# Performance work log

Hardware: AMD Instinct MI355X
Metric: run time of the kernel (lower is better)

## Reference

```python
import jax, jax.numpy as jnp
import numpy as np

B, SEQ, DIM = 4, 8192, 512
G = 32              # group_size: number of outer chunks (per source rearrange 'b (g n) d')
QK = 128            # query_key_dim
HD = QK // 4        # head_dim = 32 (used for softmax scale)
HEAD_D = 2 * HD     # per-head feature dim = 64 (h=2 heads over QK)
HID = DIM           # expansion_factor = 1.0
EPS = 1e-5


def _shift_seq(t):
    # F.pad(t, (0,0,1,-1)): prepend one zero row along axis=-2, drop last row
    pad = [(0, 0)] * (t.ndim - 2) + [(1, 0), (0, 0)]
    return jnp.pad(t, pad)[..., :-1, :]


def setup_inputs() -> dict:
    key = jax.random.key(0)
    ks = jax.random.split(key, 8)
    s = 0.02
    return {
        "x": jax.random.normal(ks[0], (B, SEQ, DIM), jnp.float32),
        "ln_g": jnp.ones((DIM,), jnp.float32),
        "ln_b": jnp.zeros((DIM,), jnp.float32),
        "w_qk": jax.random.normal(ks[1], (DIM, QK), jnp.float32) * s,
        "g4": jax.random.normal(ks[2], (4, QK), jnp.float32) * s,   # qk_offset_scale.gamma
        "b4": jnp.zeros((4, QK), jnp.float32),                       # qk_offset_scale.beta
        "g2": jax.random.normal(ks[3], (2, QK), jnp.float32) * s,   # shift_one_offset_scale.gamma
        "b2": jnp.zeros((2, QK), jnp.float32),
        "w_hidden": jax.random.normal(ks[4], (DIM, 2 * HID), jnp.float32) * s,
        "w_gate": jax.random.normal(ks[5], (DIM, HID), jnp.float32) * s,
        "w_out": jax.random.normal(ks[6], (5 * HID, DIM), jnp.float32) * s,
    }


def reference(x, ln_g, ln_b, w_qk, g4, b4, g2, b2, w_hidden, w_gate, w_out):
    b, seq, dim = x.shape
    n = seq // G  # tokens per chunk; seq chosen as multiple of G so padding = 0

    # LayerNorm
    mu = jnp.mean(x, axis=-1, keepdims=True)
    var = jnp.var(x, axis=-1, keepdims=True)
    xs = (x - mu) * jax.lax.rsqrt(var + EPS) * ln_g + ln_b

    # token shift of first half of channels (shift_tokens=True)
    half = dim // 2
    xs = jnp.concatenate([_shift_seq(xs[..., :half]), xs[..., half:]], axis=-1)

    qk = xs @ w_qk                                  # [b, seq, QK]
    qk_g = qk.reshape(b, G, n, QK)                  # 'b (g n) d -> b g n d', g outer
    qk_mean = qk_g.mean(axis=2)                     # [b, G, QK]

    # OffsetScale(heads=4) on per-chunk mean -> q_offset, k_offset, q_scale, k_scale
    offs = qk_mean[:, :, None, :] * g4 + b4         # [b, G, 4, QK]
    q_off, k_off, q_sc, k_sc = (offs[:, :, i, :] for i in range(4))

    q = qk_g * q_sc[:, :, None, :] + q_off[:, :, None, :]   # [b, G, n, QK]
    k = qk_g * k_sc[:, :, None, :] + k_off[:, :, None, :]

    # shift-by-one variants within each chunk, re-scaled + shift-one offsets
    q_s_off = qk_mean * g2[0] + b2[0]               # [b, G, QK]
    k_s_off = qk_mean * g2[1] + b2[1]
    qs = _shift_seq(q) * q_sc[:, :, None, :] + q_s_off[:, :, None, :]
    ks_ = _shift_seq(k) * k_sc[:, :, None, :] + k_s_off[:, :, None, :]

    def heads(t):  # [b,G,n,QK] -> [b,G,2,n,HEAD_D]
        return t.reshape(b, G, n, 2, HEAD_D).transpose(0, 1, 3, 2, 4)

    q_all = jnp.concatenate([heads(q), heads(qs)], axis=2)   # [b,G,4,n,64]
    k_all = jnp.concatenate([heads(k), heads(ks_)], axis=2)

    hg = xs @ w_hidden                              # [b, seq, 2*HID]
    hidden, gate = hg[..., :HID], hg[..., HID:]
    hidden_g = hidden.reshape(b, G, n, HID)

    sim = jnp.einsum('bghid,bghjd->bghij', q_all, k_all) * (HD ** -0.5)
    neg = -jnp.finfo(sim.dtype).max
    causal = jnp.triu(jnp.ones((n, n), dtype=bool), 1)  # applied unconditionally in source
    sim = jnp.where(causal, neg, sim)
    attn = jax.nn.softmax(sim, axis=-1)             # dropout=0 (eval)

    out = jnp.einsum('bghij,bgje->bghie', attn, hidden_g)   # [b,G,4,n,HID]
    gate_g = gate.reshape(b, G, n, HID)
    out = jax.nn.silu(out) * gate_g[:, :, None, :, :]
    out = out.transpose(0, 1, 3, 2, 4).reshape(b, seq, 4 * HID)  # 'b g h n e -> b (g n) (h e)'

    residual = jnp.concatenate([hidden, out], axis=-1)       # [b, seq, 5*HID]
    out = residual @ w_out                                   # [b, seq, dim]
    out = out * jax.nn.silu(xs @ w_gate)
    return out + xs
```

## Files before the change

### kernel.cpp

```cpp
#include <hip/hip_runtime.h>
#include <hip/hip_bf16.h>
#include <math.h>

#define BB 4
#define SEQ 8192
#define DIM 512
#define GG 32
#define NPG 256
#define QKD 128
#define HIDD 512

typedef unsigned short u16;
typedef unsigned int u32;

using s16x8 = __attribute__((ext_vector_type(8))) short;
using f32x4 = __attribute__((ext_vector_type(4))) float;

__device__ __forceinline__ float bf2f(u16 u) { return __uint_as_float(((u32)u) << 16); }
__device__ __forceinline__ u16 f2bf(float f) {
  u32 b = __float_as_uint(f);
  return (u16)((b + 0x7FFFu + ((b >> 16) & 1u)) >> 16);
}
__device__ __forceinline__ float silu_f(float x) { return x / (1.f + expf(-x)); }
__device__ __forceinline__ float silu_fast(float x) { return x / (1.f + __expf(-x)); }
__device__ __forceinline__ float4 fma4(float4 a, float4 b, float4 c) {
  return make_float4(a.x*b.x+c.x, a.y*b.y+c.y, a.z*b.z+c.z, a.w*b.w+c.w);
}
__device__ __forceinline__ float4 mul4(float4 a, float4 b) {
  return make_float4(a.x*b.x, a.y*b.y, a.z*b.z, a.w*b.w);
}
#define LD4(p, off) (*(const float4*)((p) + (off)))

__device__ __forceinline__ s16x8 aff8(s16x8 v, float4 s0, float4 s1, float4 o0, float4 o1) {
  union U { s16x8 x; u16 u[8]; };
  U in; in.x = v; U r;
  r.u[0] = f2bf(bf2f(in.u[0]) * s0.x + o0.x);
  r.u[1] = f2bf(bf2f(in.u[1]) * s0.y + o0.y);
  r.u[2] = f2bf(bf2f(in.u[2]) * s0.z + o0.z);
  r.u[3] = f2bf(bf2f(in.u[3]) * s0.w + o0.w);
  r.u[4] = f2bf(bf2f(in.u[4]) * s1.x + o1.x);
  r.u[5] = f2bf(bf2f(in.u[5]) * s1.y + o1.y);
  r.u[6] = f2bf(bf2f(in.u[6]) * s1.z + o1.z);
  r.u[7] = f2bf(bf2f(in.u[7]) * s1.w + o1.w);
  return r.x;
}
__device__ __forceinline__ s16x8 pack8(float4 a, float4 b) {
  union { s16x8 v; u16 u[8]; } z;
  z.u[0] = f2bf(a.x); z.u[1] = f2bf(a.y); z.u[2] = f2bf(a.z); z.u[3] = f2bf(a.w);
  z.u[4] = f2bf(b.x); z.u[5] = f2bf(b.y); z.u[6] = f2bf(b.z); z.u[7] = f2bf(b.w);
  return z.v;
}

__global__ __launch_bounds__(256) void k_ln(const float* __restrict__ x,
    const float* __restrict__ lg, const float* __restrict__ lb,
    float* __restrict__ xs, u16* __restrict__ xsb) {
  const int row = blockIdx.x;
  const int s = row & (SEQ - 1);
  const int t = threadIdx.x;
  const float* xr = x + (size_t)row * DIM;
  float v0 = xr[t], v1 = xr[t + 256];
  float sum = v0 + v1, sq = v0 * v0 + v1 * v1;
  #pragma unroll
  for (int o = 32; o; o >>= 1) { sum += __shfl_down(sum, o); sq += __shfl_down(sq, o); }
  __shared__ float sm[8];
  const int w = t >> 6;
  if ((t & 63) == 0) { sm[w] = sum; sm[4 + w] = sq; }
  __syncthreads();
  if (t == 0) {
    float S = sm[0] + sm[1] + sm[2] + sm[3];
    float Q = sm[4] + sm[5] + sm[6] + sm[7];
    float mu = S * (1.f / DIM);
    float var = Q * (1.f / DIM) - mu * mu;
    sm[0] = mu; sm[4] = rsqrtf(var + 1e-5f);
  }
  __syncthreads();
  const float mu = sm[0], rs = sm[4];
  float y0 = (v0 - mu) * rs * lg[t] + lb[t];
  float y1 = (v1 - mu) * rs * lg[t + 256] + lb[t + 256];
  xs[(size_t)row * DIM + t + 256] = y1;
  xsb[(size_t)row * DIM + t + 256] = f2bf(y1);
  if (s + 1 < SEQ) {
    xs[(size_t)(row + 1) * DIM + t] = y0;
    xsb[(size_t)(row + 1) * DIM + t] = f2bf(y0);
  }
  if (s == 0) { xs[(size_t)row * DIM + t] = 0.f; xsb[(size_t)row * DIM + t] = 0; }
}

__global__ __launch_bounds__(256) void k_trw(const float* __restrict__ src, u16* __restrict__ dst,
    int N, int dstLD, int rowOff) {
  __shared__ u16 T[64][66];
  const int t = threadIdx.x;
  const int k0 = blockIdx.x * 64, n0 = blockIdx.y * 64;
  #pragma unroll
  for (int i = 0; i < 16; ++i) {
    int idx = t + 256 * i;
    int r = idx >> 6, c = idx & 63;
    T[c][r] = f2bf(src[(size_t)(k0 + r) * N + n0 + c]);
  }
  __syncthreads();
  #pragma unroll
  for (int i = 0; i < 16; ++i) {
    int idx = t + 256 * i;
    int r = idx >> 6, c = idx & 63;
    dst[(size_t)(rowOff + n0 + r) * dstLD + k0 + c] = T[r][c];
  }
}

__global__ __launch_bounds__(256) void k_trh(const u16* __restrict__ hidt, u16* __restrict__ hidr) {
  __shared__ u16 T[64][66];
  const int t = threadIdx.x;
  const int j0 = blockIdx.x * 64;
  const int e0 = blockIdx.y * 64;
  const int bg = blockIdx.z;
  #pragma unroll
  for (int i = 0; i < 16; ++i) {
    int idx = t + 256 * i; int r = idx >> 6, c = idx & 63;
    T[c][r] = hidt[((size_t)bg * 512 + e0 + r) * 256 + j0 + c];
  }
  __syncthreads();
  #pragma unroll
  for (int i = 0; i < 16; ++i) {
    int idx = t + 256 * i; int r = idx >> 6, c = idx & 63;
    hidr[((size_t)bg * 256 + j0 + r) * 512 + e0 + c] = T[r][c];
  }
}

__global__ __launch_bounds__(256, 2) void k_gemm1m(const u16* __restrict__ xsb,
    const u16* __restrict__ w1t, u16* __restrict__ qk, u16* __restrict__ hidt,
    u16* __restrict__ gate, u16* __restrict__ xg) {
  __shared__ u16 As[2][128][72];
  __shared__ u16 Bs[2][128][72];
  const int t = threadIdx.x;
  const int blk = blockIdx.x;
  const int xcd = blk & 7;
  const int loc = blk >> 3;
  const int m0 = (xcd * 32 + loc / 13) * 128;
  const int n0 = (loc % 13) * 128;
  const int w = t >> 6, l = t & 63, lr = l & 15, lq = l >> 4;
  const int wr = (w >> 1) * 64, wc = (w & 1) * 64;
  const int sr = t >> 3;
  const int sk = (t & 7) * 8;
  f32x4 acc[4][4];
  #pragma unroll
  for (int i = 0; i < 4; ++i)
    #pragma unroll
    for (int j = 0; j < 4; ++j) acc[i][j] = (f32x4){0.f, 0.f, 0.f, 0.f};
  s16x8 rA[4], rB[4];
#define G1LOAD(T) { const int k0_ = (T) * 64;                                        \
    _Pragma("unroll")                                                                \
    for (int it = 0; it < 4; ++it) {                                                 \
      rA[it] = *(const s16x8*)(xsb + (size_t)(m0 + sr + it * 32) * 512 + k0_ + sk);  \
      rB[it] = *(const s16x8*)(w1t + (size_t)(n0 + sr + it * 32) * 512 + k0_ + sk);  \
    } }
  G1LOAD(0);
  #pragma unroll
  for (int it = 0; it < 4; ++it) {
    *(s16x8*)&As[0][sr + it * 32][sk] = rA[it];
    *(s16x8*)&Bs[0][sr + it * 32][sk] = rB[it];
  }
  G1LOAD(1);
  __syncthreads();
  for (int tt = 0; tt < 8; ++tt) {
    const int cur = tt & 1;
    if (tt + 1 < 8) {
      #pragma unroll
      for (int it = 0; it < 4; ++it) {
        *(s16x8*)&As[cur ^ 1][sr + it * 32][sk] = rA[it];
        *(s16x8*)&Bs[cur ^ 1][sr + it * 32][sk] = rB[it];
      }
      if (tt + 2 < 8) G1LOAD(tt + 2);
    }
    #pragma unroll
    for (int kk = 0; kk < 64; kk += 32) {
      s16x8 af[4], bf[4];
      #pragma unroll
      for (int fi = 0; fi < 4; ++fi) af[fi] = *(const s16x8*)&As[cur][wr + fi * 16 + lr][kk + 8 * lq];
      #pragma unroll
      for (int fj = 0; fj < 4; ++fj) bf[fj] = *(const s16x8*)&Bs[cur][wc + fj * 16 + lr][kk + 8 * lq];
      #pragma unroll
      for (int fi = 0; fi < 4; ++fi)
        #pragma unroll
        for (int fj = 0; fj < 4; ++fj)
          acc[fi][fj] = __builtin_amdgcn_mfma_f32_16x16x32_bf16(af[fi], bf[fj], acc[fi][fj], 0, 0, 0);
    }
    __syncthreads();
  }
#undef G1LOAD
  if (n0 == 0) {
    #pragma unroll
    for (int fi = 0; fi < 4; ++fi)
      #pragma unroll
      for (int fj = 0; fj < 4; ++fj) {
        const int n = wc + fj * 16 + lr;
        const int mb = m0 + wr + fi * 16 + lq * 4;
        #pragma unroll
        for (int r = 0; r < 4; ++r)
          qk[(size_t)(mb + r) * QKD + n] = f2bf(acc[fi][fj][r]);
      }
  } else if (n0 < 640) {
    const int bg = m0 >> 8;
    #pragma unroll
    for (int fi = 0; fi < 4; ++fi)
      #pragma unroll
      for (int fj = 0; fj < 4; ++fj) {
        const int e = n0 - 128 + wc + fj * 16 + lr;
        const int j0 = (m0 & 255) + wr + fi * 16 + lq * 4;
        ushort4 pk;
        pk.x = f2bf(acc[fi][fj][0]); pk.y = f2bf(acc[fi][fj][1]);
        pk.z = f2bf(acc[fi][fj][2]); pk.w = f2bf(acc[fi][fj][3]);
        *(ushort4*)(hidt + ((size_t)bg * 512 + e) * 256 + j0) = pk;
      }
  } else if (n0 < 1152) {
    #pragma unroll
    for (int fi = 0; fi < 4; ++fi)
      #pragma unroll
      for (int fj = 0; fj < 4; ++fj) {
        const int n = n0 - 640 + wc + fj * 16 + lr;
        const int mb = m0 + wr + fi * 16 + lq * 4;
        #pragma unroll
        for (int r = 0; r < 4; ++r)
          gate[(size_t)(mb + r) * HIDD + n] = f2bf(acc[fi][fj][r]);
      }
  } else {
    #pragma unroll
    for (int fi = 0; fi < 4; ++fi)
      #pragma unroll
      for (int fj = 0; fj < 4; ++fj) {
        const int n = n0 - 1152 + wc + fj * 16 + lr;
        const int mb = m0 + wr + fi * 16 + lq * 4;
        #pragma unroll
        for (int r = 0; r < 4; ++r)
          xg[(size_t)(mb + r) * HIDD + n] = f2bf(silu_f(acc[fi][fj][r]));
      }
  }
}

__global__ __launch_bounds__(128) void k_qkmean(const u16* __restrict__ qk, float* __restrict__ qm) {
  const int bg = blockIdx.x;
  const int c = threadIdx.x;
  const u16* p = qk + (size_t)bg * NPG * QKD + c;
  float s = 0.f;
  for (int i = 0; i < NPG; ++i) s += bf2f(p[(size_t)i * QKD]);
  qm[(size_t)bg * QKD + c] = s * (1.f / NPG);
}

__global__ __launch_bounds__(256, 4) void k_attn(const u16* __restrict__ qk,
    const float* __restrict__ qm, const float* __restrict__ g4, const float* __restrict__ b4,
    const float* __restrict__ g2, const float* __restrict__ b2,
    const u16* __restrict__ hidt, const u16* __restrict__ gate, u16* __restrict__ out4) {
  __shared__ u16 Vs[64][264];
  const int t = threadIdx.x;
  const int l = t & 63;
  const int h = t >> 6;
  const bool sh = (h >= 2);
  const int blk = blockIdx.x;
  const int xcd = blk & 7;
  const int bb = blk >> 3;
  const int bg = xcd * 16 + (bb >> 4);
  const int iw = 15 - (bb & 15);
  const size_t grpRow = (size_t)bg * NPG;
  const int cbase = (h & 1) << 6;
  const int lr = l & 15, lq = l >> 4;
  const int cA = cbase + 8 * lq;
  const int ntmax = iw, jtmax = iw >> 1;
  const int irow = iw * 16 + lr;
  const float* qmp = qm + bg * QKD;
  float4 qmA = LD4(qmp, cA),      qmB = LD4(qmp, cA + 4);
  float4 qmC = LD4(qmp, cA + 32), qmD = LD4(qmp, cA + 36);
  float4 qscA = fma4(qmA, LD4(g4, 2*QKD+cA),    LD4(b4, 2*QKD+cA));
  float4 qscB = fma4(qmB, LD4(g4, 2*QKD+cA+4),  LD4(b4, 2*QKD+cA+4));
  float4 qscC = fma4(qmC, LD4(g4, 2*QKD+cA+32), LD4(b4, 2*QKD+cA+32));
  float4 qscD = fma4(qmD, LD4(g4, 2*QKD+cA+36), LD4(b4, 2*QKD+cA+36));
  float4 qofA = fma4(qmA, LD4(g4, cA),      LD4(b4, cA));
  float4 qofB = fma4(qmB, LD4(g4, cA+4),    LD4(b4, cA+4));
  float4 qofC = fma4(qmC, LD4(g4, cA+32),   LD4(b4, cA+32));
  float4 qofD = fma4(qmD, LD4(g4, cA+36),   LD4(b4, cA+36));
  float4 kscA = fma4(qmA, LD4(g4, 3*QKD+cA),    LD4(b4, 3*QKD+cA));
  float4 kscB = fma4(qmB, LD4(g4, 3*QKD+cA+4),  LD4(b4, 3*QKD+cA+4));
  float4 kscC = fma4(qmC, LD4(g4, 3*QKD+cA+32), LD4(b4, 3*QKD+cA+32));
  float4 kscD = fma4(qmD, LD4(g4, 3*QKD+cA+36), LD4(b4, 3*QKD+cA+36));
  float4 kofA = fma4(qmA, LD4(g4, QKD+cA),      LD4(b4, QKD+cA));
  float4 kofB = fma4(qmB, LD4(g4, QKD+cA+4),    LD4(b4, QKD+cA+4));
  float4 kofC = fma4(qmC, LD4(g4, QKD+cA+32),   LD4(b4, QKD+cA+32));
  float4 kofD = fma4(qmD, LD4(g4, QKD+cA+36),   LD4(b4, QKD+cA+36));
  s16x8 qz0 = {0,0,0,0,0,0,0,0}, qz1 = qz0, kz0 = qz0, kz1 = qz0;
  if (sh) {
    float4 qsoA = fma4(qmA, LD4(g2, cA),    LD4(b2, cA));
    float4 qsoB = fma4(qmB, LD4(g2, cA+4),  LD4(b2, cA+4));
    float4 qsoC = fma4(qmC, LD4(g2, cA+32), LD4(b2, cA+32));
    float4 qsoD = fma4(qmD, LD4(g2, cA+36), LD4(b2, cA+36));
    float4 ksoA = fma4(qmA, LD4(g2, QKD+cA),    LD4(b2, QKD+cA));
    float4 ksoB = fma4(qmB, LD4(g2, QKD+cA+4),  LD4(b2, QKD+cA+4));
    float4 ksoC = fma4(qmC, LD4(g2, QKD+cA+32), LD4(b2, QKD+cA+32));
    float4 ksoD = fma4(qmD, LD4(g2, QKD+cA+36), LD4(b2, QKD+cA+36));
    qofA = fma4(qofA, qscA, qsoA); qofB = fma4(qofB, qscB, qsoB);
    qofC = fma4(qofC, qscC, qsoC); qofD = fma4(qofD, qscD, qsoD);
    qscA = mul4(qscA, qscA); qscB = mul4(qscB, qscB);
    qscC = mul4(qscC, qscC); qscD = mul4(qscD, qscD);
    kofA = fma4(kofA, kscA, ksoA); kofB = fma4(kofB, kscB, ksoB);
    kofC = fma4(kofC, kscC, ksoC); kofD = fma4(kofD, kscD, ksoD);
    kscA = mul4(kscA, kscA); kscB = mul4(kscB, kscB);
    kscC = mul4(kscC, kscC); kscD = mul4(kscD, kscD);
    qz0 = pack8(qsoA, qsoB); qz1 = pack8(qsoC, qsoD);
    kz0 = pack8(ksoA, ksoB); kz1 = pack8(ksoC, ksoD);
  }
  const float scl = 0.17677669529663687f;
  const int qsrc = sh ? (irow ? irow - 1 : 0) : irow;
  const u16* qrow = qk + (grpRow + qsrc) * QKD + cA;
  s16x8 qb0 = aff8(*(const s16x8*)qrow,        qscA, qscB, qofA, qofB);
  s16x8 qb1 = aff8(*(const s16x8*)(qrow + 32), qscC, qscD, qofC, qofD);
  if (sh && irow == 0) { qb0 = qz0; qb1 = qz1; }
  f32x4 sfr[16];
  #pragma unroll
  for (int nt = 0; nt < 16; ++nt) if (nt <= ntmax) {
    const int jr = nt * 16 + lr;
    const int ksrc = sh ? (jr ? jr - 1 : 0) : jr;
    const u16* kr = qk + (grpRow + ksrc) * QKD + cA;
    s16x8 ka0 = aff8(*(const s16x8*)kr,        kscA, kscB, kofA, kofB);
    s16x8 ka1 = aff8(*(const s16x8*)(kr + 32), kscC, kscD, kofC, kofD);
    if (sh && jr == 0) { ka0 = kz0; ka1 = kz1; }
    f32x4 c = {0.f, 0.f, 0.f, 0.f};
    c = __builtin_amdgcn_mfma_f32_16x16x32_bf16(ka0, qb0, c, 0, 0, 0);
    c = __builtin_amdgcn_mfma_f32_16x16x32_bf16(ka1, qb1, c, 0, 0, 0);
    sfr[nt] = c;
  }
  float mx = -3.4e38f;
  #pragma unroll
  for (int nt = 0; nt < 16; ++nt) if (nt <= ntmax) {
    #pragma unroll
    for (int r = 0; r < 4; ++r) {
      int j = nt * 16 + lq * 4 + r;
      if (j <= irow) mx = fmaxf(mx, sfr[nt][r] * scl);
    }
  }
  mx = fmaxf(mx, __shfl_xor(mx, 16));
  mx = fmaxf(mx, __shfl_xor(mx, 32));
  float sum = 0.f;
  u32 p01[16], p23[16];
  #pragma unroll
  for (int nt = 0; nt < 16; ++nt) { p01[nt] = 0u; p23[nt] = 0u; }
  #pragma unroll
  for (int nt = 0; nt < 16; ++nt) if (nt <= ntmax) {
    int j = nt * 16 + lq * 4;
    float e0 = (j + 0 <= irow) ? __expf(sfr[nt][0] * scl - mx) : 0.f;
    float e1 = (j + 1 <= irow) ? __expf(sfr[nt][1] * scl - mx) : 0.f;
    float e2 = (j + 2 <= irow) ? __expf(sfr[nt][2] * scl - mx) : 0.f;
    float e3 = (j + 3 <= irow) ? __expf(sfr[nt][3] * scl - mx) : 0.f;
    sum += (e0 + e1) + (e2 + e3);
    p01[nt] = (u32)f2bf(e0) | ((u32)f2bf(e1) << 16);
    p23[nt] = (u32)f2bf(e2) | ((u32)f2bf(e3) << 16);
  }
  sum += __shfl_xor(sum, 16);
  sum += __shfl_xor(sum, 32);
  const float inv = 1.f / sum;
  const int srcA = (l & 15) | ((l & 16) << 1);
  const int srcB = srcA + 16;
  const bool hi = (l >= 32);
  s16x8 bfr[8];
  #pragma unroll
  for (int jt = 0; jt < 8; ++jt) if (jt <= jtmax) {
    u32 a0 = __shfl((int)p01[2 * jt], srcA), a1 = __shfl((int)p23[2 * jt], srcA);
    u32 a2 = __shfl((int)p01[2 * jt], srcB), a3 = __shfl((int)p23[2 * jt], srcB);
    u32 b0 = __shfl((int)p01[2 * jt + 1], srcA), b1 = __shfl((int)p23[2 * jt + 1], srcA);
    u32 b2 = __shfl((int)p01[2 * jt + 1], srcB), b3 = __shfl((int)p23[2 * jt + 1], srcB);
    union { u32 u[4]; s16x8 v; } bb2;
    bb2.u[0] = hi ? b0 : a0; bb2.u[1] = hi ? b1 : a1;
    bb2.u[2] = hi ? b2 : a2; bb2.u[3] = hi ? b3 : a3;
    bfr[jt] = bb2.v;
  }
  const u16* vtb = hidt + (size_t)bg * (512 * 256);
  const size_t srow = grpRow + irow;
  const u16* gp = gate + srow * HIDD;
  u16* op = out4 + srow * 2048 + ((size_t)h << 9);
  for (int oct = 0; oct < 8; ++oct) {
    __syncthreads();
    const u16* src = vtb + (size_t)oct * 64 * 256;
    #pragma unroll
    for (int it = 0; it < 8; ++it) {
      int flat = it * 256 + t;
      int row = flat >> 5, col8 = (flat & 31) * 8;
      *(uint4*)&Vs[row][col8] = *(const uint4*)(src + (size_t)row * 256 + col8);
    }
    __syncthreads();
    f32x4 acc[4];
    #pragma unroll
    for (int ef = 0; ef < 4; ++ef) acc[ef] = (f32x4){0.f, 0.f, 0.f, 0.f};
    #pragma unroll
    for (int jt = 0; jt < 8; ++jt) if (jt <= jtmax) {
      __builtin_amdgcn_s_setprio(1);
      #pragma unroll
      for (int ef = 0; ef < 4; ++ef) {
        s16x8 va = *(const s16x8*)&Vs[ef * 16 + lr][jt * 32 + 8 * lq];
        acc[ef] = __builtin_amdgcn_mfma_f32_16x16x32_bf16(va, bfr[jt], acc[ef], 0, 0, 0);
      }
      __builtin_amdgcn_s_setprio(0);
    }
    #pragma unroll
    for (int ef = 0; ef < 4; ++ef) {
      const int e = oct * 64 + ef * 16 + lq * 4;
      ushort4 gu = *(const ushort4*)(gp + e);
      ushort4 ov;
      ov.x = f2bf(silu_fast(acc[ef][0] * inv) * bf2f(gu.x));
      ov.y = f2bf(silu_fast(acc[ef][1] * inv) * bf2f(gu.y));
      ov.z = f2bf(silu_fast(acc[ef][2] * inv) * bf2f(gu.z));
      ov.w = f2bf(silu_fast(acc[ef][3] * inv) * bf2f(gu.w));
      *(ushort4*)(op + e) = ov;
    }
  }
}

__global__ __launch_bounds__(256, 2) void k_gemm2m(const u16* __restrict__ hidr,
    const u16* __restrict__ out4, const u16* __restrict__ wt,
    const u16* __restrict__ xg, float* __restrict__ out) {
  __shared__ u16 As[2][128][72];
  __shared__ u16 Bs[2][128][72];
  const int t = threadIdx.x;
  const int blk = blockIdx.x;
  const int xcd = blk & 7;
  const int loc = blk >> 3;
  const int m0 = (xcd * 32 + (loc >> 2)) * 128;
  const int n0 = (loc & 3) * 128;
  const int w = t >> 6, l = t & 63, lr = l & 15, lq = l >> 4;
  const int wr = (w >> 1) * 64, wc = (w & 1) * 64;
  const int sr = t >> 3;
  const int sk = (t & 7) * 8;
  f32x4 acc[4][4];
  #pragma unroll
  for (int i = 0; i < 4; ++i)
    #pragma unroll
    for (int j = 0; j < 4; ++j) acc[i][j] = (f32x4){0.f, 0.f, 0.f, 0.f};
  s16x8 rA[4], rB[4];
#define G2LOAD(T) { const int k0_ = (T) * 64;                                        \
    const u16* ab_; size_t ald_; int ko_;                                            \
    if (k0_ < 512) { ab_ = hidr; ald_ = 512; ko_ = k0_; }                            \
    else           { ab_ = out4; ald_ = 2048; ko_ = k0_ - 512; }                     \
    _Pragma("unroll")                                                                \
    for (int it = 0; it < 4; ++it) {                                                 \
      rA[it] = *(const s16x8*)(ab_ + (size_t)(m0 + sr + it * 32) * ald_ + ko_ + sk); \
      rB[it] = *(const s16x8*)(wt + (size_t)(n0 + sr + it * 32) * 2560 + k0_ + sk);  \
    } }
  G2LOAD(0);
  #pragma unroll
  for (int it = 0; it < 4; ++it) {
    *(s16x8*)&As[0][sr + it * 32][sk] = rA[it];
    *(s16x8*)&Bs[0][sr + it * 32][sk] = rB[it];
  }
  G2LOAD(1);
  __syncthreads();
  for (int tt = 0; tt < 40; ++tt) {
    const int cur = tt & 1;
    if (tt + 1 < 40) {
      #pragma unroll
      for (int it = 0; it < 4; ++it) {
        *(s16x8*)&As[cur ^ 1][sr + it * 32][sk] = rA[it];
        *(s16x8*)&Bs[cur ^ 1][sr + it * 32][sk] = rB[it];
      }
      if (tt + 2 < 40) G2LOAD(tt + 2);
    }
    #pragma unroll
    for (int kk = 0; kk < 64; kk += 32) {
      s16x8 af[4], bf[4];
      #pragma unroll
      for (int fi = 0; fi < 4; ++fi) af[fi] = *(const s16x8*)&As[cur][wr + fi * 16 + lr][kk + 8 * lq];
      #pragma unroll
      for (int fj = 0; fj < 4; ++fj) bf[fj] = *(const s16x8*)&Bs[cur][wc + fj * 16 + lr][kk + 8 * lq];
      #pragma unroll
      for (int fi = 0; fi < 4; ++fi)
        #pragma unroll
        for (int fj = 0; fj < 4; ++fj)
          acc[fi][fj] = __builtin_amdgcn_mfma_f32_16x16x32_bf16(af[fi], bf[fj], acc[fi][fj], 0, 0, 0);
    }
    __syncthreads();
  }
#undef G2LOAD
  #pragma unroll
  for (int fi = 0; fi < 4; ++fi)
    #pragma unroll
    for (int fj = 0; fj < 4; ++fj) {
      const int n = n0 + wc + fj * 16 + lr;
      const int mb = m0 + wr + fi * 16 + lq * 4;
      #pragma unroll
      for (int r = 0; r < 4; ++r) {
        const size_t idx = (size_t)(mb + r) * DIM + n;
        out[idx] = acc[fi][fj][r] * bf2f(xg[idx]) + out[idx];
      }
    }
}

extern "C" void kernel_launch(void* const* d_in, const int* in_sizes, int n_in,
                              void* d_out, int out_size, void* d_ws, size_t ws_size,
                              hipStream_t stream) {
  const float* x        = (const float*)d_in[0];
  const float* lg       = (const float*)d_in[1];
  const float* lb       = (const float*)d_in[2];
  const float* w_qk     = (const float*)d_in[3];
  const float* g4       = (const float*)d_in[4];
  const float* b4       = (const float*)d_in[5];
  const float* g2       = (const float*)d_in[6];
  const float* b2       = (const float*)d_in[7];
  const float* w_hidden = (const float*)d_in[8];
  const float* w_gate   = (const float*)d_in[9];
  const float* w_out    = (const float*)d_in[10];
  if (ws_size < 247660544ull) return;
  char* ws = (char*)d_ws;
  float* QM   = (float*)(ws + 0);
  u16*   HIDT = (u16*)  (ws + 65536);
  u16*   GATE = (u16*)  (ws + 33619968);
  u16*   XG   = (u16*)  (ws + 67174400);
  u16*   QKb  = (u16*)  (ws + 100728832);
  u16*   W1T  = (u16*)  (ws + 109117440);
  u16*   WT   = (u16*)  (ws + 110821376);
  u16*   OUT4 = (u16*)  (ws + 113442816);
  u16*   XSB  = (u16*)  (ws + 113442816);
  u16*   HIDR = (u16*)  (ws + 33619968);
  float* XS   = (float*)d_out;
  float* OUT  = (float*)d_out;

  k_ln<<<BB * SEQ, 256, 0, stream>>>(x, lg, lb, XS, XSB);
  k_trw<<<dim3(8, 2),  256, 0, stream>>>(w_qk,     W1T, 128,  512,  0);
  k_trw<<<dim3(8, 16), 256, 0, stream>>>(w_hidden, W1T, 1024, 512,  128);
  k_trw<<<dim3(8, 8),  256, 0, stream>>>(w_gate,   W1T, 512,  512,  1152);
  k_trw<<<dim3(40, 8), 256, 0, stream>>>(w_out,    WT,  512,  2560, 0);
  k_gemm1m<<<3328, 256, 0, stream>>>(XSB, W1T, QKb, HIDT, GATE, XG);
  k_qkmean<<<BB * GG, 128, 0, stream>>>(QKb, QM);
  k_attn<<<BB * GG * 16, 256, 0, stream>>>(QKb, QM, g4, b4, g2, b2, HIDT, GATE, OUT4);
  k_trh<<<dim3(4, 8, 128), 256, 0, stream>>>(HIDT, HIDR);
  k_gemm2m<<<1024, 256, 0, stream>>>(HIDR, OUT4, WT, XG, OUT);
}
```

Measured before the change: 436.6 us.

## Load GEMM tiles directly to LDS with swizzled layout and single buffer

Replaces the register-staged, double-buffered global→LDS tile loads in both projection GEMMs with direct global_load_lds transfers into a single XOR-swizzled LDS buffer, and raises launch bounds to allow three blocks per CU. This removes the VGPR staging copies and padding, cuts LDS footprint so occupancy can rise, and relies on the swizzle to avoid bank conflicts. In exchange it drops software prefetch overlap within a block, so each tile's load now waits behind a barrier and latency hiding depends on more resident blocks.

```diff
diff --git a/kernel.cpp b/kernel.cpp
--- a/kernel.cpp
+++ b/kernel.cpp
@@ -30,6 +30,11 @@
   return make_float4(a.x*b.x, a.y*b.y, a.z*b.z, a.w*b.w);
 }
 #define LD4(p, off) (*(const float4*)((p) + (off)))
+
+__device__ __forceinline__ void gl_lds16(const u16* g, u16* l) {
+  __builtin_amdgcn_global_load_lds((const __attribute__((address_space(1))) void*)g,
+                                   (__attribute__((address_space(3))) void*)l, 16, 0, 0);
+}
 
 __device__ __forceinline__ s16x8 aff8(s16x8 v, float4 s0, float4 s1, float4 o0, float4 o1) {
   union U { s16x8 x; u16 u[8]; };
@@ -125,11 +130,11 @@
   }
 }
 
-__global__ __launch_bounds__(256, 2) void k_gemm1m(const u16* __restrict__ xsb,
+__global__ __launch_bounds__(256, 3) void k_gemm1m(const u16* __restrict__ xsb,
     const u16* __restrict__ w1t, u16* __restrict__ qk, u16* __restrict__ hidt,
     u16* __restrict__ gate, u16* __restrict__ xg) {
-  __shared__ u16 As[2][128][72];
-  __shared__ u16 Bs[2][128][72];
+  __shared__ u16 As[128 * 64];
+  __shared__ u16 Bs[128 * 64];
   const int t = threadIdx.x;
   const int blk = blockIdx.x;
   const int xcd = blk & 7;
@@ -138,45 +143,32 @@
   const int n0 = (loc % 13) * 128;
   const int w = t >> 6, l = t & 63, lr = l & 15, lq = l >> 4;
   const int wr = (w >> 1) * 64, wc = (w & 1) * 64;
-  const int sr = t >> 3;
-  const int sk = (t & 7) * 8;
+  const int rI = l >> 3;
+  const int c8 = (l & 7) ^ rI;
+  const int slotA = lq ^ (lr & 7);
+  const int slotB = (4 + lq) ^ (lr & 7);
   f32x4 acc[4][4];
   #pragma unroll
   for (int i = 0; i < 4; ++i)
     #pragma unroll
     for (int j = 0; j < 4; ++j) acc[i][j] = (f32x4){0.f, 0.f, 0.f, 0.f};
-  s16x8 rA[4], rB[4];
-#define G1LOAD(T) { const int k0_ = (T) * 64;                                        \
-    _Pragma("unroll")                                                                \
-    for (int it = 0; it < 4; ++it) {                                                 \
-      rA[it] = *(const s16x8*)(xsb + (size_t)(m0 + sr + it * 32) * 512 + k0_ + sk);  \
-      rB[it] = *(const s16x8*)(w1t + (size_t)(n0 + sr + it * 32) * 512 + k0_ + sk);  \
-    } }
-  G1LOAD(0);
-  #pragma unroll
-  for (int it = 0; it < 4; ++it) {
-    *(s16x8*)&As[0][sr + it * 32][sk] = rA[it];
-    *(s16x8*)&Bs[0][sr + it * 32][sk] = rB[it];
-  }
-  G1LOAD(1);
-  __syncthreads();
   for (int tt = 0; tt < 8; ++tt) {
-    const int cur = tt & 1;
-    if (tt + 1 < 8) {
-      #pragma unroll
-      for (int it = 0; it < 4; ++it) {
-        *(s16x8*)&As[cur ^ 1][sr + it * 32][sk] = rA[it];
-        *(s16x8*)&Bs[cur ^ 1][sr + it * 32][sk] = rB[it];
-      }
-      if (tt + 2 < 8) G1LOAD(tt + 2);
-    }
-    #pragma unroll
-    for (int kk = 0; kk < 64; kk += 32) {
+    const int k0 = tt * 64;
+    #pragma unroll
+    for (int i = 0; i < 4; ++i) {
+      const int br = w * 32 + i * 8;
+      gl_lds16(xsb + (size_t)(m0 + br + rI) * 512 + k0 + c8 * 8, &As[br * 64]);
+      gl_lds16(w1t + (size_t)(n0 + br + rI) * 512 + k0 + c8 * 8, &Bs[br * 64]);
+    }
+    __syncthreads();
+    #pragma unroll
+    for (int kk = 0; kk < 2; ++kk) {
+      const int slot = kk ? slotB : slotA;
       s16x8 af[4], bf[4];
       #pragma unroll
-      for (int fi = 0; fi < 4; ++fi) af[fi] = *(const s16x8*)&As[cur][wr + fi * 16 + lr][kk + 8 * lq];
-      #pragma unroll
-      for (int fj = 0; fj < 4; ++fj) bf[fj] = *(const s16x8*)&Bs[cur][wc + fj * 16 + lr][kk + 8 * lq];
+      for (int fi = 0; fi < 4; ++fi) af[fi] = *(const s16x8*)&As[(wr + fi * 16 + lr) * 64 + slot * 8];
+      #pragma unroll
+      for (int fj = 0; fj < 4; ++fj) bf[fj] = *(const s16x8*)&Bs[(wc + fj * 16 + lr) * 64 + slot * 8];
       #pragma unroll
       for (int fi = 0; fi < 4; ++fi)
         #pragma unroll
@@ -185,7 +177,6 @@
     }
     __syncthreads();
   }
-#undef G1LOAD
   if (n0 == 0) {
     #pragma unroll
     for (int fi = 0; fi < 4; ++fi)
@@ -409,11 +400,11 @@
   }
 }
 
-__global__ __launch_bounds__(256, 2) void k_gemm2m(const u16* __restrict__ hidr,
+__global__ __launch_bounds__(256, 3) void k_gemm2m(const u16* __restrict__ hidr,
     const u16* __restrict__ out4, const u16* __restrict__ wt,
     const u16* __restrict__ xg, float* __restrict__ out) {
-  __shared__ u16 As[2][128][72];
-  __shared__ u16 Bs[2][128][72];
+  __shared__ u16 As[128 * 64];
+  __shared__ u16 Bs[128 * 64];
   const int t = threadIdx.x;
   const int blk = blockIdx.x;
   const int xcd = blk & 7;
@@ -422,48 +413,35 @@
   const int n0 = (loc & 3) * 128;
   const int w = t >> 6, l = t & 63, lr = l & 15, lq = l >> 4;
   const int wr = (w >> 1) * 64, wc = (w & 1) * 64;
-  const int sr = t >> 3;
-  const int sk = (t & 7) * 8;
+  const int rI = l >> 3;
+  const int c8 = (l & 7) ^ rI;
+  const int slotA = lq ^ (lr & 7);
+  const int slotB = (4 + lq) ^ (lr & 7);
   f32x4 acc[4][4];
   #pragma unroll
   for (int i = 0; i < 4; ++i)
     #pragma unroll
     for (int j = 0; j < 4; ++j) acc[i][j] = (f32x4){0.f, 0.f, 0.f, 0.f};
-  s16x8 rA[4], rB[4];
-#define G2LOAD(T) { const int k0_ = (T) * 64;                                        \
-    const u16* ab_; size_t ald_; int ko_;                                            \
-    if (k0_ < 512) { ab_ = hidr; ald_ = 512; ko_ = k0_; }                            \
-    else           { ab_ = out4; ald_ = 2048; ko_ = k0_ - 512; }                     \
-    _Pragma("unroll")                                                                \
-    for (int it = 0; it < 4; ++it) {                                                 \
-      rA[it] = *(const s16x8*)(ab_ + (size_t)(m0 + sr + it * 32) * ald_ + ko_ + sk); \
-      rB[it] = *(const s16x8*)(wt + (size_t)(n0 + sr + it * 32) * 2560 + k0_ + sk);  \
-    } }
-  G2LOAD(0);
-  #pragma unroll
-  for (int it = 0; it < 4; ++it) {
-    *(s16x8*)&As[0][sr + it * 32][sk] = rA[it];
-    *(s16x8*)&Bs[0][sr + it * 32][sk] = rB[it];
-  }
-  G2LOAD(1);
-  __syncthreads();
   for (int tt = 0; tt < 40; ++tt) {
-    const int cur = tt & 1;
-    if (tt + 1 < 40) {
-      #pragma unroll
-      for (int it = 0; it < 4; ++it) {
-        *(s16x8*)&As[cur ^ 1][sr + it * 32][sk] = rA[it];
-        *(s16x8*)&Bs[cur ^ 1][sr + it * 32][sk] = rB[it];
-      }
-      if (tt + 2 < 40) G2LOAD(tt + 2);
-    }
-    #pragma unroll
-    for (int kk = 0; kk < 64; kk += 32) {
+    const int k0 = tt * 64;
+    const u16* ab; size_t ald; int ko;
+    if (k0 < 512) { ab = hidr; ald = 512;  ko = k0; }
+    else          { ab = out4; ald = 2048; ko = k0 - 512; }
+    #pragma unroll
+    for (int i = 0; i < 4; ++i) {
+      const int br = w * 32 + i * 8;
+      gl_lds16(ab + (size_t)(m0 + br + rI) * ald + ko + c8 * 8, &As[br * 64]);
+      gl_lds16(wt + (size_t)(n0 + br + rI) * 2560 + k0 + c8 * 8, &Bs[br * 64]);
+    }
+    __syncthreads();
+    #pragma unroll
+    for (int kk = 0; kk < 2; ++kk) {
+      const int slot = kk ? slotB : slotA;
       s16x8 af[4], bf[4];
       #pragma unroll
-      for (int fi = 0; fi < 4; ++fi) af[fi] = *(const s16x8*)&As[cur][wr + fi * 16 + lr][kk + 8 * lq];
-      #pragma unroll
-      for (int fj = 0; fj < 4; ++fj) bf[fj] = *(const s16x8*)&Bs[cur][wc + fj * 16 + lr][kk + 8 * lq];
+      for (int fi = 0; fi < 4; ++fi) af[fi] = *(const s16x8*)&As[(wr + fi * 16 + lr) * 64 + slot * 8];
+      #pragma unroll
+      for (int fj = 0; fj < 4; ++fj) bf[fj] = *(const s16x8*)&Bs[(wc + fj * 16 + lr) * 64 + slot * 8];
       #pragma unroll
       for (int fi = 0; fi < 4; ++fi)
         #pragma unroll
@@ -472,7 +450,6 @@
     }
     __syncthreads();
   }
-#undef G2LOAD
   #pragma unroll
   for (int fi = 0; fi < 4; ++fi)
     #pragma unroll
```

Measured after the change: 403.0 us. 1.08x faster.
